# Kernel optimization log

Hardware: AMD Instinct MI355X
Metric: run time of the kernel (lower is better)

Reference implementation:

```python
import jax, jax.numpy as jnp
import numpy as np

N = 50000
E = 800000
D = 128
L = 2


def setup_inputs() -> dict:
    key = jax.random.key(0)
    k0, k1, k2 = jax.random.split(key, 3)
    x = jax.random.normal(k0, (N, D), dtype=jnp.float32)
    edge_index = jax.random.randint(k1, (2, E), 0, N, dtype=jnp.int64)
    # GCNConv weights: one [D, D] matrix + bias per layer (dim_in -> dim_in)
    W = jax.random.normal(k2, (L, D, D), dtype=jnp.float32) * (1.0 / np.sqrt(D))
    b = jnp.zeros((L, D), dtype=jnp.float32)
    return {"x": x, "edge_index": edge_index, "W": W, "b": b}


def reference(x, edge_index, W, b):
    """Stacked GCNConv + relu (dropout is identity in eval mode).

    GCNConv: out = D^{-1/2} (A + I) D^{-1/2} (X W) + b, with self-loops added.
    """
    n = x.shape[0]
    loops = jnp.arange(n, dtype=edge_index.dtype)
    src = jnp.concatenate([edge_index[0], loops])  # [E + N]
    dst = jnp.concatenate([edge_index[1], loops])  # [E + N]
    # Degree (with self-loops) based symmetric normalization
    deg = jax.ops.segment_sum(jnp.ones_like(dst, dtype=x.dtype), dst, num_segments=n)
    dinv = jax.lax.rsqrt(deg)  # deg >= 1 thanks to self-loops
    coef = (dinv[src] * dinv[dst])[:, None]  # [E + N, 1]

    num_layers = W.shape[0]
    for i in range(num_layers):
        h = x @ W[i]  # transform first, as PyG GCNConv does
        x = jax.ops.segment_sum(h[src] * coef, dst, num_segments=n) + b[i]
        x = jax.nn.relu(x)
        # F.dropout with training=False is identity
    return x
```

## Files before the change

### kernel.cpp

```cpp
#include <hip/hip_runtime.h>
#include <hip/hip_fp16.h>


#define D 128
#define DH2 64
#define SCAN_B 256
#define WP 136

typedef _Float16 half8 __attribute__((ext_vector_type(8)));
typedef float floatx4 __attribute__((ext_vector_type(4)));


__global__ void count_kernel(const int* __restrict__ dst, int* degInt,
                             int* __restrict__ rank, int e) {
    int i = blockIdx.x * blockDim.x + threadIdx.x;
    if (i < e) rank[i] = atomicAdd(&degInt[dst[i]], 1);
}

__global__ __launch_bounds__(SCAN_B) void scanA_kernel(const int* __restrict__ degInt,
                                                       int* __restrict__ partial, int n) {
    __shared__ int red[SCAN_B / 64];
    int tid = threadIdx.x;
    int i = blockIdx.x * SCAN_B + tid;
    int c = (i < n) ? degInt[i] : 0;
    int s = c;
    for (int off = 32; off > 0; off >>= 1) s += __shfl_down(s, off, 64);
    if ((tid & 63) == 0) red[tid >> 6] = s;
    __syncthreads();
    if (tid == 0) {
        int t = 0;
#pragma unroll
        for (int w = 0; w < SCAN_B / 64; ++w) t += red[w];
        partial[blockIdx.x] = t;
    }
}

__global__ __launch_bounds__(256) void scanB_kernel(const int* __restrict__ partial,
                                                    int* __restrict__ blockoff, int nb) {
    __shared__ int sc[256];
    int tid = threadIdx.x;
    int c = (tid < nb) ? partial[tid] : 0;
    sc[tid] = c;
    __syncthreads();
    for (int off = 1; off < 256; off <<= 1) {
        int v = (tid >= off) ? sc[tid - off] : 0;
        __syncthreads();
        sc[tid] += v;
        __syncthreads();
    }
    if (tid <= nb) blockoff[tid] = (tid == 0) ? 0 : sc[tid - 1];
}

__global__ __launch_bounds__(SCAN_B) void scanC_kernel(const int* __restrict__ degInt,
                                                       const int* __restrict__ blockoff,
                                                       int* __restrict__ row_ptr,
                                                       float* __restrict__ dinv,
                                                       int n, int nb) {
    __shared__ int sc[SCAN_B];
    int tid = threadIdx.x;
    int i = blockIdx.x * SCAN_B + tid;
    int c = (i < n) ? degInt[i] : 0;
    sc[tid] = c;
    __syncthreads();
    for (int off = 1; off < SCAN_B; off <<= 1) {
        int v = (tid >= off) ? sc[tid - off] : 0;
        __syncthreads();
        sc[tid] += v;
        __syncthreads();
    }
    if (i < n) {
        int base = blockoff[blockIdx.x] + sc[tid] - c;
        row_ptr[i] = base;
        dinv[i] = rsqrtf((float)(c + 1));
    }
    if (blockIdx.x == 0 && tid == 0) row_ptr[n] = blockoff[nb];
}

__global__ void fill_kernel(const int* __restrict__ src, const int* __restrict__ dst,
                            const int* __restrict__ rank,
                            const int* __restrict__ row_ptr,
                            const float* __restrict__ dinv,
                            int2* __restrict__ recs, int e) {
    int i = blockIdx.x * blockDim.x + threadIdx.x;
    if (i < e) {
        int d = dst[i];
        int s = src[i];
        int pos = row_ptr[d] + rank[i];
        int2 rec;
        rec.x = s;
        rec.y = __float_as_int(dinv[s] * dinv[d]);
        recs[pos] = rec;
    }
}


__global__ __launch_bounds__(256) void cvtx_kernel(const float* __restrict__ X,
                                                   __half* __restrict__ Xh, int total4) {
    int i = blockIdx.x * blockDim.x + threadIdx.x;
    if (i < total4) {
        float4 v = ((const float4*)X)[i];
        __half2 p0 = __floats2half2_rn(v.x, v.y);
        __half2 p1 = __floats2half2_rn(v.z, v.w);
        uint2 pk;
        pk.x = *(unsigned int*)&p0;
        pk.y = *(unsigned int*)&p1;
        ((uint2*)Xh)[i] = pk;
    }
}

__global__ __launch_bounds__(256) void cvtw_kernel(const float* __restrict__ W,
                                                   __half* __restrict__ WhT) {
    int id = blockIdx.x * blockDim.x + threadIdx.x;
    int l = id >> 14;
    int rem = id & 16383;
    int f = rem >> 7;
    int k = rem & 127;
    WhT[id] = __float2half(W[l * 16384 + k * 128 + f]);
}


__global__ __launch_bounds__(256) void gemm_mfma_kernel(const __half* __restrict__ Xh,
                                                        const __half* __restrict__ WhT,
                                                        __half* __restrict__ Hh, int n) {
    __shared__ _Float16 wlds[128 * WP];
    const int tid = threadIdx.x;

    {
        const uint2* Wg = (const uint2*)WhT;
#pragma unroll
        for (int q = 0; q < 8; ++q) {
            int idx = tid + q * 256;
            int row = idx >> 4;
            int col8 = (idx & 15) * 8;
            const uint2* gsrc = (const uint2*)(WhT + row * 128 + col8);
            uint2 a = gsrc[0];
            uint2 b = gsrc[1];
            uint2* ldst = (uint2*)(wlds + row * WP + col8);
            ldst[0] = a;
            ldst[1] = b;
        }
    }
    __syncthreads();

    const int wave = tid >> 6;
    const int lane = tid & 63;
    const int m = lane & 15;
    const int quad = lane >> 4;

    const int node = blockIdx.x * 64 + wave * 16 + m;
    const int node_ld = node < n ? node : (n - 1);

    half8 bfr[4];
#pragma unroll
    for (int k = 0; k < 4; ++k) {
        bfr[k] = *(const half8*)(Xh + (size_t)node_ld * 128 + k * 32 + quad * 8);
    }

    floatx4 acc[8];
#pragma unroll
    for (int f = 0; f < 8; ++f) acc[f] = (floatx4){0.f, 0.f, 0.f, 0.f};

#pragma unroll
    for (int f = 0; f < 8; ++f) {
#pragma unroll
        for (int k = 0; k < 4; ++k) {
            half8 a = *(const half8*)(wlds + (f * 16 + m) * WP + k * 32 + quad * 8);
            acc[f] = __builtin_amdgcn_mfma_f32_16x16x32_f16(a, bfr[k], acc[f], 0, 0, 0);
        }
    }

    if (node < n) {
#pragma unroll
        for (int f = 0; f < 8; ++f) {
            __half2 p0 = __floats2half2_rn(acc[f][0], acc[f][1]);
            __half2 p1 = __floats2half2_rn(acc[f][2], acc[f][3]);
            uint2 pk;
            pk.x = *(unsigned int*)&p0;
            pk.y = *(unsigned int*)&p1;
            *(uint2*)(Hh + (size_t)node * 128 + f * 16 + quad * 4) = pk;
        }
    }
}


#define AB 8

__global__ __launch_bounds__(256) void agg_kernel(const __half* __restrict__ H,
                                                  const int2* __restrict__ recs,
                                                  const int* __restrict__ row_ptr,
                                                  const float* __restrict__ dinv,
                                                  const float* __restrict__ bias,
                                                  float* __restrict__ YF,
                                                  __half* __restrict__ YH,
                                                  int n, int writeHalf) {
    int wave = threadIdx.x >> 6;
    int lane = threadIdx.x & 63;
    int v = blockIdx.x * 4 + wave;
    if (v >= n) return;

    const unsigned int* H2 = (const unsigned int*)H;
    union cvt_t { unsigned int u; __half2 h; };

    float di = dinv[v];
    float selfc = di * di;
    cvt_t cv; cv.u = H2[(size_t)v * DH2 + lane];
    float2 hv = __half22float2(cv.h);
    float ax = hv.x * selfc;
    float ay = hv.y * selfc;

    int e0 = row_ptr[v];
    int e1 = row_ptr[v + 1];
    int e = e0;
    for (; e + AB <= e1; e += AB) {
        int2 r[AB]; unsigned int hu[AB];
#pragma unroll
        for (int j = 0; j < AB; ++j) r[j] = recs[e + j];
#pragma unroll
        for (int j = 0; j < AB; ++j) hu[j] = H2[(size_t)r[j].x * DH2 + lane];
#pragma unroll
        for (int j = 0; j < AB; ++j) {
            cvt_t t; t.u = hu[j];
            float2 hs = __half22float2(t.h);
            float c = __int_as_float(r[j].y);
            ax = fmaf(hs.x, c, ax);
            ay = fmaf(hs.y, c, ay);
        }
    }
    for (; e < e1; ++e) {
        int2 r = recs[e];
        cvt_t t; t.u = H2[(size_t)r.x * DH2 + lane];
        float2 hs = __half22float2(t.h);
        float c = __int_as_float(r.y);
        ax = fmaf(hs.x, c, ax);
        ay = fmaf(hs.y, c, ay);
    }
    float2 bv = ((const float2*)bias)[lane];
    float ox = ax + bv.x;
    float oy = ay + bv.y;
    ox = ox > 0.f ? ox : 0.f;
    oy = oy > 0.f ? oy : 0.f;
    if (writeHalf) {
        __half2 p = __floats2half2_rn(ox, oy);
        ((__half2*)YH)[(size_t)v * DH2 + lane] = p;
    } else {
        ((float2*)YF)[(size_t)v * DH2 + lane] = make_float2(ox, oy);
    }
}


extern "C" void kernel_launch(void* const* d_in, const int* in_sizes, int n_in,
                              void* d_out, int out_size, void* d_ws, size_t ws_size,
                              hipStream_t stream) {
    const float* x = (const float*)d_in[0];
    const int* ei = (const int*)d_in[1];
    const float* W = (const float*)d_in[2];
    const float* b = (const float*)d_in[3];
    float* out = (float*)d_out;

    const int N = in_sizes[0] / D;
    const int E = in_sizes[1] / 2;

    const int* src = ei;
    const int* dst = ei + E;

    int* wsi = (int*)d_ws;
    float* wsf = (float*)d_ws;
    const size_t o_deg  = 0;
    const size_t o_dinv = o_deg + 50000;
    const size_t o_rp   = o_dinv + 50000;
    const size_t o_part = o_rp + 50016;
    const size_t o_boff = o_part + 256;
    const size_t o_rank = o_boff + 256;
    const size_t o_rec  = o_rank + 800000;
    const size_t o_h    = o_rec + 1600000;
    const size_t o_xh   = o_h + 3200000;
    const size_t o_wht  = o_xh + 3200000;
    const size_t o_y1h  = o_wht + 16384;

    int* degInt  = wsi + o_deg;
    float* dinv  = wsf + o_dinv;
    int* row_ptr = wsi + o_rp;
    int* partial = wsi + o_part;
    int* blockoff= wsi + o_boff;
    int* rank    = wsi + o_rank;
    int2* recs   = (int2*)(wsi + o_rec);
    __half* h    = (__half*)(wsi + o_h);
    __half* xh   = (__half*)(wsi + o_xh);
    __half* wht  = (__half*)(wsi + o_wht);
    __half* y1h  = (__half*)(wsi + o_y1h);

    const int nb_e = (E + 255) / 256;
    const int nb_s = (N + SCAN_B - 1) / SCAN_B;

    hipMemsetAsync(degInt, 0, (size_t)50000 * sizeof(int), stream);
    count_kernel<<<nb_e, 256, 0, stream>>>(dst, degInt, rank, E);
    scanA_kernel<<<nb_s, SCAN_B, 0, stream>>>(degInt, partial, N);
    scanB_kernel<<<1, 256, 0, stream>>>(partial, blockoff, nb_s);
    scanC_kernel<<<nb_s, SCAN_B, 0, stream>>>(degInt, blockoff, row_ptr, dinv, N, nb_s);
    fill_kernel<<<nb_e, 256, 0, stream>>>(src, dst, rank, row_ptr, dinv, recs, E);

    cvtx_kernel<<<(N * 32 + 255) / 256, 256, 0, stream>>>(x, xh, N * 32);
    cvtw_kernel<<<128, 256, 0, stream>>>(W, wht);

    const int nb_gemm = (N + 63) / 64;
    const int nb_agg  = (N + 3) / 4;

    gemm_mfma_kernel<<<nb_gemm, 256, 0, stream>>>(xh, wht, h, N);
    agg_kernel<<<nb_agg, 256, 0, stream>>>(h, recs, row_ptr, dinv, b, nullptr, y1h, N, 1);
    gemm_mfma_kernel<<<nb_gemm, 256, 0, stream>>>(y1h, wht + 16384, h, N);
    agg_kernel<<<nb_agg, 256, 0, stream>>>(h, recs, row_ptr, dinv, b + D, out, nullptr, N, 0);
}
```

Before: 250.9 us.

## Fuse fp32-to-fp16 input conversion into GEMM and split aggregation waves across edges

Drops the separate kernel that converts x to fp16. The first GEMM now reads fp32 x directly and converts it in registers, which saves one full write and read of the fp16 copy. The aggregation kernel is also reorganised: each half-wave handles alternate edges and loads 4 halfs per lane (8-byte loads), the two partial sums are combined with a cross-half shuffle, and the scalar tail loop becomes a masked batch. This is meant to raise memory-level parallelism in the gather, at the cost of extra shuffles and some lane imbalance on odd edge counts.

```diff
diff --git a/kernel.cpp b/kernel.cpp
--- a/kernel.cpp
+++ b/kernel.cpp
@@ -3,9 +3,9 @@
 
 
 #define D 128
-#define DH2 64
 #define SCAN_B 256
 #define WP 136
+#define ABI 8
 
 typedef _Float16 half8 __attribute__((ext_vector_type(8)));
 typedef float floatx4 __attribute__((ext_vector_type(4)));
@@ -93,21 +93,6 @@
     }
 }
 
-
-__global__ __launch_bounds__(256) void cvtx_kernel(const float* __restrict__ X,
-                                                   __half* __restrict__ Xh, int total4) {
-    int i = blockIdx.x * blockDim.x + threadIdx.x;
-    if (i < total4) {
-        float4 v = ((const float4*)X)[i];
-        __half2 p0 = __floats2half2_rn(v.x, v.y);
-        __half2 p1 = __floats2half2_rn(v.z, v.w);
-        uint2 pk;
-        pk.x = *(unsigned int*)&p0;
-        pk.y = *(unsigned int*)&p1;
-        ((uint2*)Xh)[i] = pk;
-    }
-}
-
 __global__ __launch_bounds__(256) void cvtw_kernel(const float* __restrict__ W,
                                                    __half* __restrict__ WhT) {
     int id = blockIdx.x * blockDim.x + threadIdx.x;
@@ -119,26 +104,25 @@
 }
 
 
-__global__ __launch_bounds__(256) void gemm_mfma_kernel(const __half* __restrict__ Xh,
+__global__ __launch_bounds__(256) void gemm_mfma_kernel(const float* __restrict__ Xf,
+                                                        const __half* __restrict__ Xh,
                                                         const __half* __restrict__ WhT,
-                                                        __half* __restrict__ Hh, int n) {
+                                                        __half* __restrict__ Hh, int n,
+                                                        int fromFloat) {
     __shared__ _Float16 wlds[128 * WP];
     const int tid = threadIdx.x;
 
-    {
-        const uint2* Wg = (const uint2*)WhT;
-#pragma unroll
-        for (int q = 0; q < 8; ++q) {
-            int idx = tid + q * 256;
-            int row = idx >> 4;
-            int col8 = (idx & 15) * 8;
-            const uint2* gsrc = (const uint2*)(WhT + row * 128 + col8);
-            uint2 a = gsrc[0];
-            uint2 b = gsrc[1];
-            uint2* ldst = (uint2*)(wlds + row * WP + col8);
-            ldst[0] = a;
-            ldst[1] = b;
-        }
+#pragma unroll
+    for (int q = 0; q < 8; ++q) {
+        int idx = tid + q * 256;
+        int row = idx >> 4;
+        int col8 = (idx & 15) * 8;
+        const uint2* gsrc = (const uint2*)(WhT + row * 128 + col8);
+        uint2 a = gsrc[0];
+        uint2 b = gsrc[1];
+        uint2* ldst = (uint2*)(wlds + row * WP + col8);
+        ldst[0] = a;
+        ldst[1] = b;
     }
     __syncthreads();
 
@@ -151,9 +135,24 @@
     const int node_ld = node < n ? node : (n - 1);
 
     half8 bfr[4];
-#pragma unroll
-    for (int k = 0; k < 4; ++k) {
-        bfr[k] = *(const half8*)(Xh + (size_t)node_ld * 128 + k * 32 + quad * 8);
+    if (fromFloat) {
+#pragma unroll
+        for (int k = 0; k < 4; ++k) {
+            const float4* p = (const float4*)(Xf + (size_t)node_ld * 128 + k * 32 + quad * 8);
+            float4 lo = p[0];
+            float4 hi = p[1];
+            half8 h;
+            h[0] = (_Float16)lo.x; h[1] = (_Float16)lo.y;
+            h[2] = (_Float16)lo.z; h[3] = (_Float16)lo.w;
+            h[4] = (_Float16)hi.x; h[5] = (_Float16)hi.y;
+            h[6] = (_Float16)hi.z; h[7] = (_Float16)hi.w;
+            bfr[k] = h;
+        }
+    } else {
+#pragma unroll
+        for (int k = 0; k < 4; ++k) {
+            bfr[k] = *(const half8*)(Xh + (size_t)node_ld * 128 + k * 32 + quad * 8);
+        }
     }
 
     floatx4 acc[8];
@@ -183,7 +182,13 @@
 }
 
 
-#define AB 8
+__device__ inline float4 unpack4(uint2 u) {
+    union { unsigned int x; __half2 h; } a, b;
+    a.x = u.x; b.x = u.y;
+    float2 f0 = __half22float2(a.h);
+    float2 f1 = __half22float2(b.h);
+    return make_float4(f0.x, f0.y, f1.x, f1.y);
+}
 
 __global__ __launch_bounds__(256) void agg_kernel(const __half* __restrict__ H,
                                                   const int2* __restrict__ recs,
@@ -198,52 +203,83 @@
     int v = blockIdx.x * 4 + wave;
     if (v >= n) return;
 
-    const unsigned int* H2 = (const unsigned int*)H;
-    union cvt_t { unsigned int u; __half2 h; };
+    const int sub = lane >> 5;
+    const int fl  = lane & 31;
+    const uint2* H4 = (const uint2*)H;
 
     float di = dinv[v];
-    float selfc = di * di;
-    cvt_t cv; cv.u = H2[(size_t)v * DH2 + lane];
-    float2 hv = __half22float2(cv.h);
-    float ax = hv.x * selfc;
-    float ay = hv.y * selfc;
+    float selfc = (sub == 0) ? di * di : 0.f;
+    float4 hself = unpack4(H4[(size_t)v * 32 + fl]);
+    float ax = hself.x * selfc;
+    float ay = hself.y * selfc;
+    float az = hself.z * selfc;
+    float aw = hself.w * selfc;
 
     int e0 = row_ptr[v];
     int e1 = row_ptr[v + 1];
     int e = e0;
-    for (; e + AB <= e1; e += AB) {
-        int2 r[AB]; unsigned int hu[AB];
-#pragma unroll
-        for (int j = 0; j < AB; ++j) r[j] = recs[e + j];
-#pragma unroll
-        for (int j = 0; j < AB; ++j) hu[j] = H2[(size_t)r[j].x * DH2 + lane];
-#pragma unroll
-        for (int j = 0; j < AB; ++j) {
-            cvt_t t; t.u = hu[j];
-            float2 hs = __half22float2(t.h);
+    for (; e + 2 * ABI <= e1; e += 2 * ABI) {
+        int2 r[ABI]; uint2 hu[ABI];
+#pragma unroll
+        for (int j = 0; j < ABI; ++j) r[j] = recs[e + 2 * j + sub];
+#pragma unroll
+        for (int j = 0; j < ABI; ++j) hu[j] = H4[(size_t)r[j].x * 32 + fl];
+#pragma unroll
+        for (int j = 0; j < ABI; ++j) {
             float c = __int_as_float(r[j].y);
+            float4 hs = unpack4(hu[j]);
             ax = fmaf(hs.x, c, ax);
             ay = fmaf(hs.y, c, ay);
-        }
-    }
-    for (; e < e1; ++e) {
-        int2 r = recs[e];
-        cvt_t t; t.u = H2[(size_t)r.x * DH2 + lane];
-        float2 hs = __half22float2(t.h);
-        float c = __int_as_float(r.y);
-        ax = fmaf(hs.x, c, ax);
-        ay = fmaf(hs.y, c, ay);
-    }
-    float2 bv = ((const float2*)bias)[lane];
-    float ox = ax + bv.x;
-    float oy = ay + bv.y;
-    ox = ox > 0.f ? ox : 0.f;
-    oy = oy > 0.f ? oy : 0.f;
-    if (writeHalf) {
-        __half2 p = __floats2half2_rn(ox, oy);
-        ((__half2*)YH)[(size_t)v * DH2 + lane] = p;
-    } else {
-        ((float2*)YF)[(size_t)v * DH2 + lane] = make_float2(ox, oy);
+            az = fmaf(hs.z, c, az);
+            aw = fmaf(hs.w, c, aw);
+        }
+    }
+    if (e < e1) {
+        int2 r[ABI]; uint2 hu[ABI]; bool act[ABI];
+#pragma unroll
+        for (int j = 0; j < ABI; ++j) {
+            int idx = e + 2 * j + sub;
+            act[j] = idx < e1;
+            if (act[j]) r[j] = recs[idx];
+        }
+#pragma unroll
+        for (int j = 0; j < ABI; ++j) {
+            if (act[j]) hu[j] = H4[(size_t)r[j].x * 32 + fl];
+        }
+#pragma unroll
+        for (int j = 0; j < ABI; ++j) {
+            if (act[j]) {
+                float c = __int_as_float(r[j].y);
+                float4 hs = unpack4(hu[j]);
+                ax = fmaf(hs.x, c, ax);
+                ay = fmaf(hs.y, c, ay);
+                az = fmaf(hs.z, c, az);
+                aw = fmaf(hs.w, c, aw);
+            }
+        }
+    }
+    ax += __shfl_xor(ax, 32);
+    ay += __shfl_xor(ay, 32);
+    az += __shfl_xor(az, 32);
+    aw += __shfl_xor(aw, 32);
+
+    float4 bv = ((const float4*)bias)[fl];
+    float ox = fmaxf(ax + bv.x, 0.f);
+    float oy = fmaxf(ay + bv.y, 0.f);
+    float oz = fmaxf(az + bv.z, 0.f);
+    float ow = fmaxf(aw + bv.w, 0.f);
+
+    if (sub == 0) {
+        if (writeHalf) {
+            __half2 p0 = __floats2half2_rn(ox, oy);
+            __half2 p1 = __floats2half2_rn(oz, ow);
+            uint2 pk;
+            pk.x = *(unsigned int*)&p0;
+            pk.y = *(unsigned int*)&p1;
+            ((uint2*)YH)[(size_t)v * 32 + fl] = pk;
+        } else {
+            ((float4*)YF)[(size_t)v * 32 + fl] = make_float4(ox, oy, oz, ow);
+        }
     }
 }
 
@@ -273,8 +309,7 @@
     const size_t o_rank = o_boff + 256;
     const size_t o_rec  = o_rank + 800000;
     const size_t o_h    = o_rec + 1600000;
-    const size_t o_xh   = o_h + 3200000;
-    const size_t o_wht  = o_xh + 3200000;
+    const size_t o_wht  = o_h + 3200000;
     const size_t o_y1h  = o_wht + 16384;
 
     int* degInt  = wsi + o_deg;
@@ -285,7 +320,6 @@
     int* rank    = wsi + o_rank;
     int2* recs   = (int2*)(wsi + o_rec);
     __half* h    = (__half*)(wsi + o_h);
-    __half* xh   = (__half*)(wsi + o_xh);
     __half* wht  = (__half*)(wsi + o_wht);
     __half* y1h  = (__half*)(wsi + o_y1h);
 
@@ -298,15 +332,13 @@
     scanB_kernel<<<1, 256, 0, stream>>>(partial, blockoff, nb_s);
     scanC_kernel<<<nb_s, SCAN_B, 0, stream>>>(degInt, blockoff, row_ptr, dinv, N, nb_s);
     fill_kernel<<<nb_e, 256, 0, stream>>>(src, dst, rank, row_ptr, dinv, recs, E);
-
-    cvtx_kernel<<<(N * 32 + 255) / 256, 256, 0, stream>>>(x, xh, N * 32);
     cvtw_kernel<<<128, 256, 0, stream>>>(W, wht);
 
     const int nb_gemm = (N + 63) / 64;
     const int nb_agg  = (N + 3) / 4;
 
-    gemm_mfma_kernel<<<nb_gemm, 256, 0, stream>>>(xh, wht, h, N);
+    gemm_mfma_kernel<<<nb_gemm, 256, 0, stream>>>(x, nullptr, wht, h, N, 1);
     agg_kernel<<<nb_agg, 256, 0, stream>>>(h, recs, row_ptr, dinv, b, nullptr, y1h, N, 1);
-    gemm_mfma_kernel<<<nb_gemm, 256, 0, stream>>>(y1h, wht + 16384, h, N);
+    gemm_mfma_kernel<<<nb_gemm, 256, 0, stream>>>(nullptr, y1h, wht + 16384, h, N, 0);
     agg_kernel<<<nb_agg, 256, 0, stream>>>(h, recs, row_ptr, dinv, b + D, out, nullptr, N, 0);
 }
```

After: 243.2 us. -3.1%, faster.
